# Optimization experiments

Measured on AMD Instinct MI355X. Metric: run time of the kernel, lower is better.

## Reference

```python
import jax, jax.numpy as jnp
import numpy as np

S, P, H, E = 32, 32, 128, 64        # scenes, peds/scene, h_dim, embedding_dim
B1, B2 = 512, 1024                  # mlp_pre_pool hidden, bottleneck_dim
M1 = 1024                           # decoder mlp hidden
N = S * P
T = 12                              # seq_len (decode horizon)
BN_INV = 1.0 / np.sqrt(1.0 + 1e-5)  # eval-mode BatchNorm, running mean=0 var=1


def setup_inputs() -> dict:
    key = jax.random.key(0)
    ks = jax.random.split(key, 32)
    rn = lambda k, sh, s=0.05: jax.random.normal(k, sh, dtype=jnp.float32) * s
    inp = {
        'last_pos': rn(ks[0], (N, 2), 1.0),
        'last_pos_rel': rn(ks[1], (N, 2), 1.0),
        'h0': rn(ks[2], (N, H), 0.1),
        'c0': rn(ks[3], (N, H), 0.1),
        'seq_start_end': jnp.stack([jnp.arange(S) * P, (jnp.arange(S) + 1) * P], 1).astype(jnp.int32),
        # decoder spatial embedding Linear(2, E)
        'emb_W': rn(ks[4], (E, 2)), 'emb_b': rn(ks[5], (E,)),
        # LSTM (torch gate order i,f,g,o)
        'lstm_Wih': rn(ks[6], (4 * H, E)), 'lstm_Whh': rn(ks[7], (4 * H, H)),
        'lstm_bih': rn(ks[8], (4 * H,)), 'lstm_bhh': rn(ks[9], (4 * H,)),
        # hidden2pos Linear(H, 2)
        'pos_W': rn(ks[10], (2, H)), 'pos_b': rn(ks[11], (2,)),
        # pool_net spatial embedding Linear(2, E)
        'sp_W': rn(ks[12], (E, 2)), 'sp_b': rn(ks[13], (E,)),
        # mlp_pre_pool: Linear(E+H, 512)+BN+ReLU, Linear(512, 1024)+BN+ReLU
        'pp1_W': rn(ks[14], (B1, E + H)), 'pp1_b': rn(ks[15], (B1,)),
        'pp1_g': 1.0 + rn(ks[16], (B1,)), 'pp1_be': rn(ks[17], (B1,)),
        'pp2_W': rn(ks[18], (B2, B1)), 'pp2_b': rn(ks[19], (B2,)),
        'pp2_g': 1.0 + rn(ks[20], (B2,)), 'pp2_be': rn(ks[21], (B2,)),
        # decoder mlp: Linear(H+1024, 1024)+BN+ReLU, Linear(1024, H)+BN+ReLU
        'm1_W': rn(ks[22], (M1, H + B2)), 'm1_b': rn(ks[23], (M1,)),
        'm1_g': 1.0 + rn(ks[24], (M1,)), 'm1_be': rn(ks[25], (M1,)),
        'm2_W': rn(ks[26], (H, M1)), 'm2_b': rn(ks[27], (H,)),
        'm2_g': 1.0 + rn(ks[28], (H,)), 'm2_be': rn(ks[29], (H,)),
    }
    return inp


def _bn(x, g, b):
    return x * BN_INV * g + b


def reference(last_pos, last_pos_rel, h0, c0, seq_start_end,
              emb_W, emb_b, lstm_Wih, lstm_Whh, lstm_bih, lstm_bhh,
              pos_W, pos_b, sp_W, sp_b,
              pp1_W, pp1_b, pp1_g, pp1_be, pp2_W, pp2_b, pp2_g, pp2_be,
              m1_W, m1_b, m1_g, m1_be, m2_W, m2_b, m2_g, m2_be):
    # seq_start_end encodes uniform scenes of size P; pooling is done per scene.
    def step(carry, _):
        h, c, lp, din = carry  # h,c:[N,H]  lp:[N,2]  din:[N,E]
        gates = din @ lstm_Wih.T + lstm_bih + h @ lstm_Whh.T + lstm_bhh
        i, f, g_, o = jnp.split(gates, 4, axis=-1)
        c2 = jax.nn.sigmoid(f) * c + jax.nn.sigmoid(i) * jnp.tanh(g_)
        h2 = jax.nn.sigmoid(o) * jnp.tanh(c2)
        rel_pos = h2 @ pos_W.T + pos_b          # [N,2]
        curr = rel_pos + lp                     # [N,2]
        # ---- PoolHiddenNet: per-scene all-pairs gather -> MLP -> max ----
        ps = curr.reshape(S, P, 2)
        rel = ps[:, None, :, :] - ps[:, :, None, :]   # [s,i,j] = pos_j - pos_i
        rel = rel / jnp.maximum(jnp.linalg.norm(rel, axis=-1, keepdims=True), 1e-12)
        emb = rel @ sp_W.T + sp_b                      # [S,P,P,E]
        hj = jnp.broadcast_to(h2.reshape(S, 1, P, H), (S, P, P, H))
        x = jnp.concatenate([emb, hj], -1)             # [S,P,P,E+H]
        x = jax.nn.relu(_bn(x @ pp1_W.T + pp1_b, pp1_g, pp1_be))
        x = jax.nn.relu(_bn(x @ pp2_W.T + pp2_b, pp2_g, pp2_be))
        pool = x.max(axis=2).reshape(N, B2)            # max over neighbours j
        # ---- hidden refinement MLP ----
        dh = jnp.concatenate([h2, pool], 1)
        dh = jax.nn.relu(_bn(dh @ m1_W.T + m1_b, m1_g, m1_be))
        dh = jax.nn.relu(_bn(dh @ m2_W.T + m2_b, m2_g, m2_be))
        din2 = rel_pos @ emb_W.T + emb_b
        return (dh, c2, curr, din2), rel_pos

    din0 = last_pos_rel @ emb_W.T + emb_b
    _, preds = jax.lax.scan(step, (h0, c0, last_pos, din0), None, length=T)
    return preds  # [T, N, 2] predicted relative displacements
```

## Files before the change

### kernel.cpp

```cpp
#include <hip/hip_runtime.h>
#include <hip/hip_bf16.h>
#include <math.h>

#define DEVFN __device__ __forceinline__

constexpr float BN_INV = 0.99999500003749971f;

DEVFN float sigm(float x) { return 1.0f / (1.0f + expf(-x)); }

DEVFN unsigned short f2bf(float f) {
    __hip_bfloat16 b = __float2bfloat16(f);
    return *reinterpret_cast<unsigned short*>(&b);
}
DEVFN float bf2f(unsigned short u) {
    unsigned int x = ((unsigned int)u) << 16;
    return *reinterpret_cast<float*>(&x);
}
DEVFN void splitf(float v, unsigned short& h, unsigned short& l) {
    h = f2bf(v);
    l = f2bf(v - bf2f(h));
}
DEVFN unsigned int pack2(unsigned short a, unsigned short b) {
    return (unsigned int)a | ((unsigned int)b << 16);
}
DEVFN unsigned int packsplit(float v) {
    unsigned short h, l;
    splitf(v, h, l);
    return pack2(h, l);
}

typedef __attribute__((ext_vector_type(8))) short short8;
typedef __attribute__((ext_vector_type(4))) float f32x4;

DEVFN void unzip16(unsigned short* dh, unsigned short* dl,
                   uint4 a0, uint4 a1, uint4 a2, uint4 a3) {
    uint4 h0, h1, l0, l1;
    h0.x = (a0.x & 0xffffu) | (a0.y << 16); l0.x = (a0.x >> 16) | (a0.y & 0xffff0000u);
    h0.y = (a0.z & 0xffffu) | (a0.w << 16); l0.y = (a0.z >> 16) | (a0.w & 0xffff0000u);
    h0.z = (a1.x & 0xffffu) | (a1.y << 16); l0.z = (a1.x >> 16) | (a1.y & 0xffff0000u);
    h0.w = (a1.z & 0xffffu) | (a1.w << 16); l0.w = (a1.z >> 16) | (a1.w & 0xffff0000u);
    h1.x = (a2.x & 0xffffu) | (a2.y << 16); l1.x = (a2.x >> 16) | (a2.y & 0xffff0000u);
    h1.y = (a2.z & 0xffffu) | (a2.w << 16); l1.y = (a2.z >> 16) | (a2.w & 0xffff0000u);
    h1.z = (a3.x & 0xffffu) | (a3.y << 16); l1.z = (a3.x >> 16) | (a3.y & 0xffff0000u);
    h1.w = (a3.z & 0xffffu) | (a3.w << 16); l1.w = (a3.z >> 16) | (a3.w & 0xffff0000u);
    *(uint4*)dh = h0; *(uint4*)(dh + 8) = h1;
    *(uint4*)dl = l0; *(uint4*)(dl + 8) = l1;
}

#define ASYNC_COPY16(gsrc, ldst)                                                            \
    __builtin_amdgcn_global_load_lds((const __attribute__((address_space(1))) unsigned int*)(gsrc), \
                                     (__attribute__((address_space(3))) unsigned int*)(ldst), 16, 0, 0)


__global__ void pre_misc(
    const float* __restrict__ Wih, const float* __restrict__ Whh,
    const float* __restrict__ bih, const float* __restrict__ bhh,
    float* __restrict__ WgT, float* __restrict__ bg,
    const float* __restrict__ pp1W, const float* __restrict__ pp1g,
    float* __restrict__ Wh1T,
    const float* __restrict__ spW, const float* __restrict__ spb,
    const float* __restrict__ pp1b, const float* __restrict__ pp1be,
    float* __restrict__ Mp, float* __restrict__ c1,
    const float* __restrict__ lp, const float* __restrict__ lpr,
    const float* __restrict__ h0, const float* __restrict__ c0,
    const float* __restrict__ embW, const float* __restrict__ embb,
    float* __restrict__ h_st, float* __restrict__ c_st,
    float* __restrict__ curr, float* __restrict__ din) {
    int bid = blockIdx.x, t = threadIdx.x;
    if (bid < 384) {
        int idx = bid * 256 + t;
        int k = idx >> 9, tt = idx & 511;
        WgT[idx] = (k < 64) ? Wih[tt * 64 + k] : Whh[tt * 128 + (k - 64)];
        if (idx < 512) bg[idx] = bih[idx] + bhh[idx];
    } else if (bid < 640) {
        int idx = (bid - 384) * 256 + t;
        int h = idx >> 9, k = idx & 511;
        Wh1T[idx] = pp1W[k * 192 + 64 + h] * (BN_INV * pp1g[k]);
    } else if (bid < 642) {
        int k = (bid - 640) * 256 + t;
        float m0 = 0.f, m1 = 0.f, c0v = 0.f;
        for (int e = 0; e < 64; e++) {
            float w = pp1W[k * 192 + e];
            m0 += spW[e * 2] * w; m1 += spW[e * 2 + 1] * w; c0v += spb[e] * w;
        }
        float s = BN_INV * pp1g[k];
        Mp[k] = m0 * s; Mp[512 + k] = m1 * s;
        c1[k] = (c0v + pp1b[k]) * s + pp1be[k];
    } else {
        int idx = (bid - 642) * 256 + t;
        h_st[idx] = h0[idx];
        c_st[idx] = c0[idx];
        if (idx < 1024 * 2) curr[idx] = lp[idx];
        if (idx < 1024 * 64) {
            int n = idx >> 6, e = idx & 63;
            din[idx] = fmaf(lpr[n * 2], embW[e * 2], fmaf(lpr[n * 2 + 1], embW[e * 2 + 1], embb[e]));
        }
    }
}

__global__ void pre_w(
    const float* __restrict__ pp2W, const float* __restrict__ pp2b,
    const float* __restrict__ pp2g, const float* __restrict__ pp2be,
    unsigned short* __restrict__ W2bf, float* __restrict__ c2v, int swz,
    const float* __restrict__ m1W, const float* __restrict__ m1b,
    const float* __restrict__ m1g, const float* __restrict__ m1be,
    unsigned int* __restrict__ M1p, float* __restrict__ cm1,
    const float* __restrict__ m2W, const float* __restrict__ m2b,
    const float* __restrict__ m2g, const float* __restrict__ m2be,
    unsigned int* __restrict__ M2p, float* __restrict__ cm2) {
    int bid = blockIdx.x, t = threadIdx.x;
    if (bid < 2048) {
        int idx = bid * 256 + t;
        int ko = idx >> 9, k = idx & 511;
        float s = BN_INV * pp2g[ko];
        int outk = swz ? ((k & ~63) | ((((k >> 3) & 7) ^ (ko & 7)) << 3) | (k & 7)) : k;
        W2bf[(ko << 9) + outk] = f2bf(pp2W[idx] * s);
        if (idx < 1024) c2v[idx] = pp2b[idx] * s + pp2be[idx];
    } else if (bid < 6656) {
        int idx = (bid - 2048) * 256 + t;
        int ko = idx / 1152;
        float s = BN_INV * m1g[ko];
        M1p[idx] = packsplit(m1W[idx] * s);
        if (idx < 1024) {
            float s2 = BN_INV * m1g[idx];
            cm1[idx] = m1b[idx] * s2 + m1be[idx];
        }
    } else {
        int idx = (bid - 6656) * 256 + t;
        int ko = idx >> 10;
        float s = BN_INV * m2g[ko];
        M2p[idx] = packsplit(m2W[idx] * s);
        if (idx < 128) {
            float s2 = BN_INV * m2g[idx];
            cm2[idx] = m2b[idx] * s2 + m2be[idx];
        }
    }
}


__global__ __launch_bounds__(512) void k_lstm(
    const float* __restrict__ WgT, const float* __restrict__ bg,
    float* __restrict__ h_st, float* __restrict__ c_st,
    float* __restrict__ din, float* __restrict__ curr,
    unsigned int* __restrict__ h2p,
    const float* __restrict__ posW, const float* __restrict__ posb,
    const float* __restrict__ embW, const float* __restrict__ embb,
    const float* __restrict__ Wh1T, const float* __restrict__ c1,
    float* __restrict__ Hp, int doHp,
    float* __restrict__ preds) {
    int n0 = blockIdx.x << 2;
    int t = threadIdx.x;
    __shared__ float xs[4][256];
    __shared__ float gates[4][512];
    __shared__ float h2s[4][128];
    __shared__ float rp[4][2];
#pragma unroll
    for (int u = 0; u < 2; u++) {
        int lin = t + (u << 9);
        int r = lin >> 8, k = lin & 255;
        float v = 0.f;
        if (k < 64) v = din[(n0 + r) * 64 + k];
        else if (k < 192) v = h_st[(n0 + r) * 128 + (k - 64)];
        xs[r][k] = v;
    }
    __syncthreads();
    float a0 = bg[t], a1 = a0, a2 = a0, a3 = a0;
#pragma unroll 4
    for (int k = 0; k < 192; k++) {
        float w = WgT[(k << 9) + t];
        a0 = fmaf(xs[0][k], w, a0);
        a1 = fmaf(xs[1][k], w, a1);
        a2 = fmaf(xs[2][k], w, a2);
        a3 = fmaf(xs[3][k], w, a3);
    }
    gates[0][t] = a0; gates[1][t] = a1; gates[2][t] = a2; gates[3][t] = a3;
    __syncthreads();
    {
        int r = t >> 7, hx = t & 127;
        float ig = sigm(gates[r][hx]);
        float fg = sigm(gates[r][128 + hx]);
        float gg = tanhf(gates[r][256 + hx]);
        float og = sigm(gates[r][384 + hx]);
        float c2 = fmaf(fg, c_st[(n0 + r) * 128 + hx], ig * gg);
        float h2 = og * tanhf(c2);
        c_st[(n0 + r) * 128 + hx] = c2;
        h2p[(n0 + r) * 128 + hx] = packsplit(h2);
        h2s[r][hx] = h2;
    }
    __syncthreads();
    int wv = t >> 6, l = t & 63;
    if (wv < 4) {
        float p0 = fmaf(h2s[wv][l], posW[l], h2s[wv][l + 64] * posW[l + 64]);
        float p1 = fmaf(h2s[wv][l], posW[128 + l], h2s[wv][l + 64] * posW[192 + l]);
#pragma unroll
        for (int off = 32; off > 0; off >>= 1) {
            p0 += __shfl_down(p0, off, 64);
            p1 += __shfl_down(p1, off, 64);
        }
        if (l == 0) { rp[wv][0] = p0 + posb[0]; rp[wv][1] = p1 + posb[1]; }
    }
    __syncthreads();
    if (t < 256) {
        int r = t >> 6, e = t & 63;
        float r0 = rp[r][0], r1 = rp[r][1];
        din[(n0 + r) * 64 + e] = fmaf(r0, embW[e * 2], fmaf(r1, embW[e * 2 + 1], embb[e]));
        if (e == 0) {
            preds[(n0 + r) * 2] = r0; preds[(n0 + r) * 2 + 1] = r1;
            curr[(n0 + r) * 2] += r0; curr[(n0 + r) * 2 + 1] += r1;
        }
    }
    if (doHp) {
        float cc = c1[t];
        float q0 = cc, q1 = cc, q2 = cc, q3 = cc;
#pragma unroll 4
        for (int h = 0; h < 128; h++) {
            float w = Wh1T[(h << 9) + t];
            q0 = fmaf(h2s[0][h], w, q0);
            q1 = fmaf(h2s[1][h], w, q1);
            q2 = fmaf(h2s[2][h], w, q2);
            q3 = fmaf(h2s[3][h], w, q3);
        }
        Hp[((n0 + 0) << 9) + t] = q0;
        Hp[((n0 + 1) << 9) + t] = q1;
        Hp[((n0 + 2) << 9) + t] = q2;
        Hp[((n0 + 3) << 9) + t] = q3;
    }
}

__global__ __launch_bounds__(256) void k_x1(
    const float* __restrict__ Hp, const float* __restrict__ Mp,
    const float* __restrict__ curr, unsigned short* __restrict__ x1g) {
    int bid = blockIdx.x;
    int c = bid & 7, q = bid >> 3;
    int i = q & 31, g = q >> 5;
    int s = (g << 3) + c;
    int si = (s << 5) + i;
    int t = threadIdx.x;
    __shared__ float rx[32], ry[32];
    __shared__ float m0s[512], m1s[512];
    for (int u = t; u < 512; u += 256) { m0s[u] = Mp[u]; m1s[u] = Mp[512 + u]; }
    if (t < 32) {
        int jg = (s << 5) + t;
        float dx = curr[jg * 2] - curr[si * 2];
        float dy = curr[jg * 2 + 1] - curr[si * 2 + 1];
        float den = fmaxf(sqrtf(dx * dx + dy * dy), 1e-12f);
        rx[t] = dx / den; ry[t] = dy / den;
    }
    __syncthreads();
    int j = t >> 3, c8 = t & 7;
    float rxv = rx[j], ryv = ry[j];
    const float* hp = Hp + (((s << 5) + j) << 9);
    unsigned short* op = x1g + ((size_t)((si << 5) + j) << 9);
    int swz = (c8 ^ (j & 7)) << 3;
#pragma unroll
    for (int kt = 0; kt < 512; kt += 64) {
        int k = kt + (c8 << 3);
        float4 ha = *(const float4*)(hp + k);
        float4 hb = *(const float4*)(hp + k + 4);
        uint4 o;
        o.x = pack2(f2bf(fmaxf(fmaf(rxv, m0s[k + 0], fmaf(ryv, m1s[k + 0], ha.x)), 0.f)),
                    f2bf(fmaxf(fmaf(rxv, m0s[k + 1], fmaf(ryv, m1s[k + 1], ha.y)), 0.f)));
        o.y = pack2(f2bf(fmaxf(fmaf(rxv, m0s[k + 2], fmaf(ryv, m1s[k + 2], ha.z)), 0.f)),
                    f2bf(fmaxf(fmaf(rxv, m0s[k + 3], fmaf(ryv, m1s[k + 3], ha.w)), 0.f)));
        o.z = pack2(f2bf(fmaxf(fmaf(rxv, m0s[k + 4], fmaf(ryv, m1s[k + 4], hb.x)), 0.f)),
                    f2bf(fmaxf(fmaf(rxv, m0s[k + 5], fmaf(ryv, m1s[k + 5], hb.y)), 0.f)));
        o.w = pack2(f2bf(fmaxf(fmaf(rxv, m0s[k + 6], fmaf(ryv, m1s[k + 6], hb.z)), 0.f)),
                    f2bf(fmaxf(fmaf(rxv, m0s[k + 7], fmaf(ryv, m1s[k + 7], hb.w)), 0.f)));
        *(uint4*)(op + kt + swz) = o;
    }
}

__global__ __launch_bounds__(1024, 4) void k_pool_g(
    const unsigned short* __restrict__ x1g, const unsigned short* __restrict__ W2bf,
    const float* __restrict__ c2v,
    unsigned int* __restrict__ poolp) {
    int bid = blockIdx.x;
    int c = bid & 7, q = bid >> 3;
    int inner = q & 15, g = q >> 4;
    int s = (g << 3) + c;
    int rb = inner >> 2;
    int koB = (inner & 3) << 8;
    int t = threadIdx.x;
    int lane = t & 63, wv = t >> 6;
    int quad = lane >> 4, l15 = lane & 15;
    int wr = wv >> 2, wc = wv & 3;
    int qrow = wr << 6, qcol = wc << 6;
    __shared__ unsigned short As[2][256 * 64];
    __shared__ unsigned short Bs[2][256 * 64];
    f32x4 acc[4][4];
#pragma unroll
    for (int a = 0; a < 4; a++)
#pragma unroll
        for (int b = 0; b < 4; b++) acc[a][b] = (f32x4){0.f, 0.f, 0.f, 0.f};

    int rlane = lane >> 3;
    int clane = (lane & 7) << 3;
    const unsigned short* gA = x1g + (size_t)((s << 10) + (rb << 8) + (wv << 4) + rlane) * 512 + clane;
    const unsigned short* gB = W2bf + (size_t)(koB + (wv << 4) + rlane) * 512 + clane;
    const unsigned short* pa0 = &As[0][((qrow + l15) << 6) + ((quad ^ (l15 & 7)) << 3)];
    const unsigned short* pb0 = &Bs[0][((qcol + l15) << 6) + ((quad ^ (l15 & 7)) << 3)];
    const unsigned short* pa1 = &As[0][((qrow + l15) << 6) + (((4 + quad) ^ (l15 & 7)) << 3)];
    const unsigned short* pb1 = &Bs[0][((qcol + l15) << 6) + (((4 + quad) ^ (l15 & 7)) << 3)];

#define POOL_STAGE(kt, buf)                                           \
    do {                                                              \
        unsigned short* lA = &As[buf][wv << 10];                      \
        unsigned short* lB = &Bs[buf][wv << 10];                      \
        ASYNC_COPY16(gA + (kt), lA);                                  \
        ASYNC_COPY16(gA + (kt) + 8 * 512, lA + (8 << 6));             \
        ASYNC_COPY16(gB + (kt), lB);                                  \
        ASYNC_COPY16(gB + (kt) + 8 * 512, lB + (8 << 6));             \
    } while (0)

    POOL_STAGE(0, 0);
    __syncthreads();
    for (int i = 0; i < 8; i++) {
        if (i < 7) POOL_STAGE((i + 1) << 6, (i + 1) & 1);
        int off = (i & 1) << 14;
        short8 aF[4], bF[4];
#pragma unroll
        for (int a = 0; a < 4; a++) aF[a] = *(const short8*)(pa0 + off + (a << 10));
#pragma unroll
        for (int b = 0; b < 4; b++) bF[b] = *(const short8*)(pb0 + off + (b << 10));
#pragma unroll
        for (int a = 0; a < 4; a++)
#pragma unroll
            for (int b = 0; b < 4; b++)
                acc[a][b] = __builtin_amdgcn_mfma_f32_16x16x32_bf16(aF[a], bF[b], acc[a][b], 0, 0, 0);
#pragma unroll
        for (int a = 0; a < 4; a++) aF[a] = *(const short8*)(pa1 + off + (a << 10));
#pragma unroll
        for (int b = 0; b < 4; b++) bF[b] = *(const short8*)(pb1 + off + (b << 10));
#pragma unroll
        for (int a = 0; a < 4; a++)
#pragma unroll
            for (int b = 0; b < 4; b++)
                acc[a][b] = __builtin_amdgcn_mfma_f32_16x16x32_bf16(aF[a], bF[b], acc[a][b], 0, 0, 0);
        __syncthreads();
    }
#undef POOL_STAGE

    float mx0[4], mx1[4];
#pragma unroll
    for (int b = 0; b < 4; b++) {
        float m = acc[0][b].x;
#pragma unroll
        for (int a = 0; a < 2; a++) {
            m = fmaxf(m, acc[a][b].x); m = fmaxf(m, acc[a][b].y);
            m = fmaxf(m, acc[a][b].z); m = fmaxf(m, acc[a][b].w);
        }
        m = fmaxf(m, __shfl_xor(m, 16));
        m = fmaxf(m, __shfl_xor(m, 32));
        mx0[b] = m;
        float n = acc[2][b].x;
#pragma unroll
        for (int a = 2; a < 4; a++) {
            n = fmaxf(n, acc[a][b].x); n = fmaxf(n, acc[a][b].y);
            n = fmaxf(n, acc[a][b].z); n = fmaxf(n, acc[a][b].w);
        }
        n = fmaxf(n, __shfl_xor(n, 16));
        n = fmaxf(n, __shfl_xor(n, 32));
        mx1[b] = n;
    }
    float v0 = (quad == 0) ? mx0[0] : (quad == 1) ? mx0[1] : (quad == 2) ? mx0[2] : mx0[3];
    float v1 = (quad == 0) ? mx1[0] : (quad == 1) ? mx1[1] : (quad == 2) ? mx1[2] : mx1[3];
    int col = koB + qcol + (quad << 4) + l15;
    int i0 = (rb << 3) + (wr << 1);
    int si0 = (s << 5) + i0;
    float bias = c2v[col];
    poolp[si0 * 1024 + col] = packsplit(fmaxf(v0 + bias, 0.f));
    poolp[(si0 + 1) * 1024 + col] = packsplit(fmaxf(v1 + bias, 0.f));
}

__global__ __launch_bounds__(256) void k_pool_mfma(
    const float* __restrict__ Hp, const float* __restrict__ Mp,
    const unsigned short* __restrict__ W2bf,
    const float* __restrict__ c2v, const float* __restrict__ curr,
    unsigned int* __restrict__ poolp) {
    int s = blockIdx.z;
    int rb = blockIdx.y;
    int koBase = blockIdx.x << 7;
    int t = threadIdx.x;
    int lane = t & 63, wv = t >> 6;
    int quad = lane >> 4, l15 = lane & 15;
    int qrow = (wv >> 1) << 6;
    int qcol = (wv & 1) << 6;

    __shared__ unsigned short As[128 * 40];
    __shared__ unsigned short Bs[128 * 40];
    __shared__ float rx[128], ry[128];

    if (t < 128) {
        int iL = t >> 5, j = t & 31;
        int ig = (s << 5) + (rb << 2) + iL;
        int jg = (s << 5) + j;
        float dx = curr[jg * 2] - curr[ig * 2];
        float dy = curr[jg * 2 + 1] - curr[ig * 2 + 1];
        float den = fmaxf(sqrtf(dx * dx + dy * dy), 1e-12f);
        rx[t] = dx / den; ry[t] = dy / den;
    }
    __syncthreads();

    f32x4 acc[4][4];
#pragma unroll
    for (int a = 0; a < 4; a++)
#pragma unroll
        for (int b = 0; b < 4; b++) acc[a][b] = (f32x4){0.f, 0.f, 0.f, 0.f};

    int r0 = t >> 3, c4 = (t & 7) << 2;
    int bn = t >> 1, bk = (t & 1) << 4;

    for (int kt = 0; kt < 512; kt += 32) {
#pragma unroll
        for (int p = 0; p < 4; p++) {
            int rr = r0 + (p << 5);
            int j = rr & 31;
            int kg = kt + c4;
            float4 hv = *(const float4*)(Hp + (((s << 5) + j) << 9) + kg);
            float4 m0 = *(const float4*)(Mp + kg);
            float4 m1 = *(const float4*)(Mp + 512 + kg);
            float rxv = rx[rr], ryv = ry[rr];
            float v0 = fmaxf(fmaf(rxv, m0.x, fmaf(ryv, m1.x, hv.x)), 0.f);
            float v1 = fmaxf(fmaf(rxv, m0.y, fmaf(ryv, m1.y, hv.y)), 0.f);
            float v2 = fmaxf(fmaf(rxv, m0.z, fmaf(ryv, m1.z, hv.z)), 0.f);
            float v3 = fmaxf(fmaf(rxv, m0.w, fmaf(ryv, m1.w, hv.w)), 0.f);
            unsigned int u0 = pack2(f2bf(v0), f2bf(v1));
            unsigned int u1 = pack2(f2bf(v2), f2bf(v3));
            *(uint2*)(&As[rr * 40 + c4]) = make_uint2(u0, u1);
        }
        {
            const unsigned short* src = W2bf + (((koBase + bn) << 9) + kt + bk);
            uint4 w0 = *(const uint4*)src;
            uint4 w1 = *(const uint4*)(src + 8);
            *(uint4*)(&Bs[bn * 40 + bk]) = w0;
            *(uint4*)(&Bs[bn * 40 + bk + 8]) = w1;
        }
        __syncthreads();
        short8 bF[4];
#pragma unroll
        for (int b = 0; b < 4; b++)
            bF[b] = *(const short8*)(&Bs[(qcol + (b << 4) + l15) * 40 + (quad << 3)]);
#pragma unroll
        for (int a = 0; a < 4; a++) {
            short8 aF = *(const short8*)(&As[(qrow + (a << 4) + l15) * 40 + (quad << 3)]);
#pragma unroll
            for (int b = 0; b < 4; b++)
                acc[a][b] = __builtin_amdgcn_mfma_f32_16x16x32_bf16(aF, bF[b], acc[a][b], 0, 0, 0);
        }
        __syncthreads();
    }

    float mx0[4], mx1[4];
#pragma unroll
    for (int b = 0; b < 4; b++) {
        float m = acc[0][b].x;
#pragma unroll
        for (int a = 0; a < 2; a++) {
            m = fmaxf(m, acc[a][b].x); m = fmaxf(m, acc[a][b].y);
            m = fmaxf(m, acc[a][b].z); m = fmaxf(m, acc[a][b].w);
        }
        m = fmaxf(m, __shfl_xor(m, 16));
        m = fmaxf(m, __shfl_xor(m, 32));
        mx0[b] = m;
        float n = acc[2][b].x;
#pragma unroll
        for (int a = 2; a < 4; a++) {
            n = fmaxf(n, acc[a][b].x); n = fmaxf(n, acc[a][b].y);
            n = fmaxf(n, acc[a][b].z); n = fmaxf(n, acc[a][b].w);
        }
        n = fmaxf(n, __shfl_xor(n, 16));
        n = fmaxf(n, __shfl_xor(n, 32));
        mx1[b] = n;
    }
    float v0 = (quad == 0) ? mx0[0] : (quad == 1) ? mx0[1] : (quad == 2) ? mx0[2] : mx0[3];
    float v1 = (quad == 0) ? mx1[0] : (quad == 1) ? mx1[1] : (quad == 2) ? mx1[2] : mx1[3];
    int col = koBase + qcol + (quad << 4) + l15;
    int i0 = (rb << 2) + ((wv >> 1) << 1);
    int si0 = (s << 5) + i0;
    float bias = c2v[col];
    poolp[si0 * 1024 + col] = packsplit(fmaxf(v0 + bias, 0.f));
    poolp[(si0 + 1) * 1024 + col] = packsplit(fmaxf(v1 + bias, 0.f));
}

__global__ __launch_bounds__(256) void k_m1_mfma(
    const unsigned int* __restrict__ h2p, const unsigned int* __restrict__ poolp,
    const unsigned int* __restrict__ M1p, const float* __restrict__ cm1,
    unsigned int* __restrict__ dh1p) {
    int bid = blockIdx.x;
    int c = bid & 7, q = bid >> 3;
    int kg = (c << 1) | (q >> 4);
    int rowg = q & 15;
    int rowBase = rowg << 6;
    int koBase = kg << 6;
    int t = threadIdx.x;
    int lane = t & 63, wv = t >> 6;
    int quad = lane >> 4, l15 = lane & 15;
    int qrow = (wv >> 1) << 5, qcol = (wv & 1) << 5;
    __shared__ unsigned short Ah[64 * 72], Al[64 * 72], Bh[64 * 72], Bl[64 * 72];
    f32x4 acc[2][2];
#pragma unroll
    for (int a = 0; a < 2; a++)
#pragma unroll
        for (int b = 0; b < 2; b++) acc[a][b] = (f32x4){0.f, 0.f, 0.f, 0.f};

    int ar = t >> 2, ak = (t & 3) << 4;

    for (int kt = 0; kt < 1152; kt += 64) {
        {
            const unsigned int* srcA = (kt < 128)
                ? h2p + (rowBase + ar) * 128 + kt + ak
                : poolp + (rowBase + ar) * 1024 + (kt - 128) + ak;
            uint4 a0 = ((const uint4*)srcA)[0];
            uint4 a1 = ((const uint4*)srcA)[1];
            uint4 a2 = ((const uint4*)srcA)[2];
            uint4 a3 = ((const uint4*)srcA)[3];
            const unsigned int* srcB = M1p + (koBase + ar) * 1152 + kt + ak;
            uint4 b0 = ((const uint4*)srcB)[0];
            uint4 b1 = ((const uint4*)srcB)[1];
            uint4 b2 = ((const uint4*)srcB)[2];
            uint4 b3 = ((const uint4*)srcB)[3];
            unzip16(&Ah[ar * 72 + ak], &Al[ar * 72 + ak], a0, a1, a2, a3);
            unzip16(&Bh[ar * 72 + ak], &Bl[ar * 72 + ak], b0, b1, b2, b3);
        }
        __syncthreads();
#pragma unroll
        for (int kk2 = 0; kk2 < 2; kk2++) {
            int kc = ((kk2 << 2) | quad) << 3;
            short8 bH[2], bL[2];
#pragma unroll
            for (int b = 0; b < 2; b++) {
                int boff = (qcol + (b << 4) + l15) * 72 + kc;
                bH[b] = *(const short8*)(&Bh[boff]);
                bL[b] = *(const short8*)(&Bl[boff]);
            }
#pragma unroll
            for (int a = 0; a < 2; a++) {
                int aoff = (qrow + (a << 4) + l15) * 72 + kc;
                short8 aH = *(const short8*)(&Ah[aoff]);
                short8 aL = *(const short8*)(&Al[aoff]);
#pragma unroll
                for (int b = 0; b < 2; b++) {
                    acc[a][b] = __builtin_amdgcn_mfma_f32_16x16x32_bf16(aH, bH[b], acc[a][b], 0, 0, 0);
                    acc[a][b] = __builtin_amdgcn_mfma_f32_16x16x32_bf16(aH, bL[b], acc[a][b], 0, 0, 0);
                    acc[a][b] = __builtin_amdgcn_mfma_f32_16x16x32_bf16(aL, bH[b], acc[a][b], 0, 0, 0);
                }
            }
        }
        __syncthreads();
    }
#pragma unroll
    for (int b = 0; b < 2; b++) {
        int col = koBase + qcol + (b << 4) + l15;
        float bias = cm1[col];
#pragma unroll
        for (int a = 0; a < 2; a++) {
#pragma unroll
            for (int rg = 0; rg < 4; rg++) {
                int row = rowBase + qrow + (a << 4) + (quad << 2) + rg;
                dh1p[row * 1024 + col] = packsplit(fmaxf(acc[a][b][rg] + bias, 0.f));
            }
        }
    }
}

__global__ __launch_bounds__(256) void k_m2_mfma(
    const unsigned int* __restrict__ dh1p, const unsigned int* __restrict__ M2p,
    const float* __restrict__ cm2, float* __restrict__ h_st) {
    int rowBase = blockIdx.x << 5;
    int t = threadIdx.x;
    int lane = t & 63, wv = t >> 6;
    int quad = lane >> 4, l15 = lane & 15;
    int qrow = (wv >> 1) << 4;
    int qcol = (wv & 1) << 6;
    __shared__ unsigned short Ah[32 * 40], Al[32 * 40], Bh[128 * 40], Bl[128 * 40];
    f32x4 acc[4];
#pragma unroll
    for (int b = 0; b < 4; b++) acc[b] = (f32x4){0.f, 0.f, 0.f, 0.f};

    int ar = t >> 3, ak = (t & 7) << 2;
    int br = t >> 1, bk = (t & 1) << 4;

    for (int kt = 0; kt < 1024; kt += 32) {
        {
            uint4 av = *(const uint4*)(dh1p + (rowBase + ar) * 1024 + kt + ak);
            uint2 hi = make_uint2((av.x & 0xffffu) | (av.y << 16),
                                  (av.z & 0xffffu) | (av.w << 16));
            uint2 lo = make_uint2((av.x >> 16) | (av.y & 0xffff0000u),
                                  (av.z >> 16) | (av.w & 0xffff0000u));
            *(uint2*)&Ah[ar * 40 + ak] = hi;
            *(uint2*)&Al[ar * 40 + ak] = lo;
        }
        {
            const unsigned int* srcB = M2p + br * 1024 + kt + bk;
            uint4 b0 = ((const uint4*)srcB)[0];
            uint4 b1 = ((const uint4*)srcB)[1];
            uint4 b2 = ((const uint4*)srcB)[2];
            uint4 b3 = ((const uint4*)srcB)[3];
            unzip16(&Bh[br * 40 + bk], &Bl[br * 40 + bk], b0, b1, b2, b3);
        }
        __syncthreads();
        {
            int aoff = (qrow + l15) * 40 + (quad << 3);
            short8 aH = *(const short8*)(&Ah[aoff]);
            short8 aL = *(const short8*)(&Al[aoff]);
#pragma unroll
            for (int b = 0; b < 4; b++) {
                int boff = (qcol + (b << 4) + l15) * 40 + (quad << 3);
                short8 bH = *(const short8*)(&Bh[boff]);
                short8 bL = *(const short8*)(&Bl[boff]);
                acc[b] = __builtin_amdgcn_mfma_f32_16x16x32_bf16(aH, bH, acc[b], 0, 0, 0);
                acc[b] = __builtin_amdgcn_mfma_f32_16x16x32_bf16(aH, bL, acc[b], 0, 0, 0);
                acc[b] = __builtin_amdgcn_mfma_f32_16x16x32_bf16(aL, bH, acc[b], 0, 0, 0);
            }
        }
        __syncthreads();
    }
#pragma unroll
    for (int b = 0; b < 4; b++) {
        int col = qcol + (b << 4) + l15;
        float bias = cm2[col];
#pragma unroll
        for (int rg = 0; rg < 4; rg++) {
            int row = rowBase + qrow + (quad << 2) + rg;
            h_st[row * 128 + col] = fmaxf(acc[b][rg] + bias, 0.f);
        }
    }
}


extern "C" void kernel_launch(void* const* d_in, const int* in_sizes, int n_in,
                              void* d_out, int out_size, void* d_ws, size_t ws_size,
                              hipStream_t stream) {
    const float* last_pos     = (const float*)d_in[0];
    const float* last_pos_rel = (const float*)d_in[1];
    const float* h0   = (const float*)d_in[2];
    const float* c0   = (const float*)d_in[3];
    const float* emb_W = (const float*)d_in[5];
    const float* emb_b = (const float*)d_in[6];
    const float* lstm_Wih = (const float*)d_in[7];
    const float* lstm_Whh = (const float*)d_in[8];
    const float* lstm_bih = (const float*)d_in[9];
    const float* lstm_bhh = (const float*)d_in[10];
    const float* pos_W = (const float*)d_in[11];
    const float* pos_b = (const float*)d_in[12];
    const float* sp_W  = (const float*)d_in[13];
    const float* sp_b  = (const float*)d_in[14];
    const float* pp1_W = (const float*)d_in[15];
    const float* pp1_b = (const float*)d_in[16];
    const float* pp1_g = (const float*)d_in[17];
    const float* pp1_be= (const float*)d_in[18];
    const float* pp2_W = (const float*)d_in[19];
    const float* pp2_b = (const float*)d_in[20];
    const float* pp2_g = (const float*)d_in[21];
    const float* pp2_be= (const float*)d_in[22];
    const float* m1_W  = (const float*)d_in[23];
    const float* m1_b  = (const float*)d_in[24];
    const float* m1_g  = (const float*)d_in[25];
    const float* m1_be = (const float*)d_in[26];
    const float* m2_W  = (const float*)d_in[27];
    const float* m2_b  = (const float*)d_in[28];
    const float* m2_g  = (const float*)d_in[29];
    const float* m2_be = (const float*)d_in[30];
    float* out = (float*)d_out;

    float* p = (float*)d_ws;
    float* WgT  = p; p += 192 * 512;
    float* bg   = p; p += 512;
    float* Wh1T = p; p += 128 * 512;
    float* Mp   = p; p += 2 * 512;
    float* c1   = p; p += 512;
    unsigned short* W2bf = (unsigned short*)p; p += 512 * 1024 / 2;
    float* c2v  = p; p += 1024;
    unsigned int* M1p = (unsigned int*)p; p += 1024 * 1152;
    float* cm1  = p; p += 1024;
    unsigned int* M2p = (unsigned int*)p; p += 128 * 1024;
    float* cm2  = p; p += 128;
    float* h_st = p; p += 1024 * 128;
    float* c_st = p; p += 1024 * 128;
    unsigned int* h2p = (unsigned int*)p; p += 1024 * 128;
    float* curr = p; p += 1024 * 2;
    float* din  = p; p += 1024 * 64;
    float* Hp   = p; p += 1024 * 512;
    unsigned int* poolp = (unsigned int*)p; p += 1024 * 1024;
    unsigned int* dh1p = (unsigned int*)p; p += 1024 * 1024;
    unsigned short* x1g = (unsigned short*)p;
    size_t need = (size_t)((char*)(x1g + (size_t)32768 * 512) - (char*)d_ws);
    int big = (ws_size >= need) ? 1 : 0;

    pre_misc<<<1154, 256, 0, stream>>>(lstm_Wih, lstm_Whh, lstm_bih, lstm_bhh, WgT, bg,
                                       pp1_W, pp1_g, Wh1T,
                                       sp_W, sp_b, pp1_b, pp1_be, Mp, c1,
                                       last_pos, last_pos_rel, h0, c0, emb_W, emb_b,
                                       h_st, c_st, curr, din);
    pre_w<<<7168, 256, 0, stream>>>(pp2_W, pp2_b, pp2_g, pp2_be, W2bf, c2v, big,
                                    m1_W, m1_b, m1_g, m1_be, M1p, cm1,
                                    m2_W, m2_b, m2_g, m2_be, M2p, cm2);

    for (int t = 0; t < 12; t++) {
        k_lstm<<<256, 512, 0, stream>>>(WgT, bg, h_st, c_st, din, curr, h2p,
                                        pos_W, pos_b, emb_W, emb_b,
                                        Wh1T, c1, Hp, (t < 11) ? 1 : 0, out + t * 2048);
        if (t == 11) break;
        if (big) {
            k_x1<<<1024, 256, 0, stream>>>(Hp, Mp, curr, x1g);
            k_pool_g<<<512, 1024, 0, stream>>>(x1g, W2bf, c2v, poolp);
        } else {
            k_pool_mfma<<<dim3(8, 8, 32), 256, 0, stream>>>(Hp, Mp, W2bf, c2v, curr, poolp);
        }
        k_m1_mfma<<<256, 256, 0, stream>>>(h2p, poolp, M1p, cm1, dh1p);
        k_m2_mfma<<<32, 256, 0, stream>>>(dh1p, M2p, cm2, h_st);
    }
}
```

Baseline: 1.484 ms.

## Fuse pairwise first-layer activation build into pooled GEMM kernel

Removes the separate k_x1 kernel that materialised the full bf16 pairwise activation tensor in global memory, and instead builds each A tile from Hp, Mp and relative positions inside the pool GEMM while B tiles are fetched asynchronously. This avoids writing and then re-reading a large intermediate each step, at the cost of ALU work and global reads inside the GEMM main loop that are not overlapped by async copies. The fallback small-workspace path is dropped, and the m1 kernel grid is changed from a swizzled 1D mapping to a plain 2D grid.

```diff
diff --git a/kernel.cpp b/kernel.cpp
--- a/kernel.cpp
+++ b/kernel.cpp
@@ -101,7 +101,7 @@
 __global__ void pre_w(
     const float* __restrict__ pp2W, const float* __restrict__ pp2b,
     const float* __restrict__ pp2g, const float* __restrict__ pp2be,
-    unsigned short* __restrict__ W2bf, float* __restrict__ c2v, int swz,
+    unsigned short* __restrict__ W2bf, float* __restrict__ c2v,
     const float* __restrict__ m1W, const float* __restrict__ m1b,
     const float* __restrict__ m1g, const float* __restrict__ m1be,
     unsigned int* __restrict__ M1p, float* __restrict__ cm1,
@@ -113,7 +113,7 @@
         int idx = bid * 256 + t;
         int ko = idx >> 9, k = idx & 511;
         float s = BN_INV * pp2g[ko];
-        int outk = swz ? ((k & ~63) | ((((k >> 3) & 7) ^ (ko & 7)) << 3) | (k & 7)) : k;
+        int outk = (k & ~63) | ((((k >> 3) & 7) ^ (ko & 7)) << 3) | (k & 7);
         W2bf[(ko << 9) + outk] = f2bf(pp2W[idx] * s);
         if (idx < 1024) c2v[idx] = pp2b[idx] * s + pp2be[idx];
     } else if (bid < 6656) {
@@ -227,51 +227,9 @@
     }
 }
 
-__global__ __launch_bounds__(256) void k_x1(
+__global__ __launch_bounds__(1024, 4) void k_pool_f(
     const float* __restrict__ Hp, const float* __restrict__ Mp,
-    const float* __restrict__ curr, unsigned short* __restrict__ x1g) {
-    int bid = blockIdx.x;
-    int c = bid & 7, q = bid >> 3;
-    int i = q & 31, g = q >> 5;
-    int s = (g << 3) + c;
-    int si = (s << 5) + i;
-    int t = threadIdx.x;
-    __shared__ float rx[32], ry[32];
-    __shared__ float m0s[512], m1s[512];
-    for (int u = t; u < 512; u += 256) { m0s[u] = Mp[u]; m1s[u] = Mp[512 + u]; }
-    if (t < 32) {
-        int jg = (s << 5) + t;
-        float dx = curr[jg * 2] - curr[si * 2];
-        float dy = curr[jg * 2 + 1] - curr[si * 2 + 1];
-        float den = fmaxf(sqrtf(dx * dx + dy * dy), 1e-12f);
-        rx[t] = dx / den; ry[t] = dy / den;
-    }
-    __syncthreads();
-    int j = t >> 3, c8 = t & 7;
-    float rxv = rx[j], ryv = ry[j];
-    const float* hp = Hp + (((s << 5) + j) << 9);
-    unsigned short* op = x1g + ((size_t)((si << 5) + j) << 9);
-    int swz = (c8 ^ (j & 7)) << 3;
-#pragma unroll
-    for (int kt = 0; kt < 512; kt += 64) {
-        int k = kt + (c8 << 3);
-        float4 ha = *(const float4*)(hp + k);
-        float4 hb = *(const float4*)(hp + k + 4);
-        uint4 o;
-        o.x = pack2(f2bf(fmaxf(fmaf(rxv, m0s[k + 0], fmaf(ryv, m1s[k + 0], ha.x)), 0.f)),
-                    f2bf(fmaxf(fmaf(rxv, m0s[k + 1], fmaf(ryv, m1s[k + 1], ha.y)), 0.f)));
-        o.y = pack2(f2bf(fmaxf(fmaf(rxv, m0s[k + 2], fmaf(ryv, m1s[k + 2], ha.z)), 0.f)),
-                    f2bf(fmaxf(fmaf(rxv, m0s[k + 3], fmaf(ryv, m1s[k + 3], ha.w)), 0.f)));
-        o.z = pack2(f2bf(fmaxf(fmaf(rxv, m0s[k + 4], fmaf(ryv, m1s[k + 4], hb.x)), 0.f)),
-                    f2bf(fmaxf(fmaf(rxv, m0s[k + 5], fmaf(ryv, m1s[k + 5], hb.y)), 0.f)));
-        o.w = pack2(f2bf(fmaxf(fmaf(rxv, m0s[k + 6], fmaf(ryv, m1s[k + 6], hb.z)), 0.f)),
-                    f2bf(fmaxf(fmaf(rxv, m0s[k + 7], fmaf(ryv, m1s[k + 7], hb.w)), 0.f)));
-        *(uint4*)(op + kt + swz) = o;
-    }
-}
-
-__global__ __launch_bounds__(1024, 4) void k_pool_g(
-    const unsigned short* __restrict__ x1g, const unsigned short* __restrict__ W2bf,
+    const float* __restrict__ curr, const unsigned short* __restrict__ W2bf,
     const float* __restrict__ c2v,
     unsigned int* __restrict__ poolp) {
     int bid = blockIdx.x;
@@ -287,35 +245,95 @@
     int qrow = wr << 6, qcol = wc << 6;
     __shared__ unsigned short As[2][256 * 64];
     __shared__ unsigned short Bs[2][256 * 64];
+    __shared__ float rxs[256], rys[256];
+
+    if (t < 256) {
+        int iL = t >> 5, j = t & 31;
+        int ig = (s << 5) + (rb << 3) + iL;
+        int jg = (s << 5) + j;
+        float dx = curr[jg * 2] - curr[ig * 2];
+        float dy = curr[jg * 2 + 1] - curr[ig * 2 + 1];
+        float den = fmaxf(sqrtf(dx * dx + dy * dy), 1e-12f);
+        rxs[t] = dx / den; rys[t] = dy / den;
+    }
+    __syncthreads();
+
     f32x4 acc[4][4];
 #pragma unroll
     for (int a = 0; a < 4; a++)
 #pragma unroll
         for (int b = 0; b < 4; b++) acc[a][b] = (f32x4){0.f, 0.f, 0.f, 0.f};
+
+    int br_ = t >> 2;
+    int bj = br_ & 31;
+    int k0 = (t & 3) << 4;
+    int c0 = (t & 3) << 1;
+    int sw0 = ((c0 ^ (br_ & 7)) << 3);
+    int sw1 = (((c0 + 1) ^ (br_ & 7)) << 3);
+    const float* hpRow = Hp + (((s << 5) + bj) << 9);
+    float rxv = rxs[br_], ryv = rys[br_];
 
     int rlane = lane >> 3;
     int clane = (lane & 7) << 3;
-    const unsigned short* gA = x1g + (size_t)((s << 10) + (rb << 8) + (wv << 4) + rlane) * 512 + clane;
     const unsigned short* gB = W2bf + (size_t)(koB + (wv << 4) + rlane) * 512 + clane;
+
     const unsigned short* pa0 = &As[0][((qrow + l15) << 6) + ((quad ^ (l15 & 7)) << 3)];
     const unsigned short* pb0 = &Bs[0][((qcol + l15) << 6) + ((quad ^ (l15 & 7)) << 3)];
     const unsigned short* pa1 = &As[0][((qrow + l15) << 6) + (((4 + quad) ^ (l15 & 7)) << 3)];
     const unsigned short* pb1 = &Bs[0][((qcol + l15) << 6) + (((4 + quad) ^ (l15 & 7)) << 3)];
 
-#define POOL_STAGE(kt, buf)                                           \
+#define BUILD_A(kt, buf)                                                        \
+    do {                                                                        \
+        unsigned short* baseA = &As[buf][br_ << 6];                             \
+        int kk = (kt) + k0;                                                     \
+        float4 h0 = *(const float4*)(hpRow + kk);                               \
+        float4 h1 = *(const float4*)(hpRow + kk + 4);                           \
+        float4 h2v = *(const float4*)(hpRow + kk + 8);                          \
+        float4 h3 = *(const float4*)(hpRow + kk + 12);                          \
+        float4 p0 = *(const float4*)(Mp + kk);                                  \
+        float4 p1 = *(const float4*)(Mp + kk + 4);                              \
+        float4 p2 = *(const float4*)(Mp + kk + 8);                              \
+        float4 p3 = *(const float4*)(Mp + kk + 12);                             \
+        float4 q0 = *(const float4*)(Mp + 512 + kk);                            \
+        float4 q1 = *(const float4*)(Mp + 512 + kk + 4);                        \
+        float4 q2 = *(const float4*)(Mp + 512 + kk + 8);                        \
+        float4 q3 = *(const float4*)(Mp + 512 + kk + 12);                       \
+        uint4 o0, o1;                                                           \
+        o0.x = pack2(f2bf(fmaxf(fmaf(rxv, p0.x, fmaf(ryv, q0.x, h0.x)), 0.f)),  \
+                     f2bf(fmaxf(fmaf(rxv, p0.y, fmaf(ryv, q0.y, h0.y)), 0.f))); \
+        o0.y = pack2(f2bf(fmaxf(fmaf(rxv, p0.z, fmaf(ryv, q0.z, h0.z)), 0.f)),  \
+                     f2bf(fmaxf(fmaf(rxv, p0.w, fmaf(ryv, q0.w, h0.w)), 0.f))); \
+        o0.z = pack2(f2bf(fmaxf(fmaf(rxv, p1.x, fmaf(ryv, q1.x, h1.x)), 0.f)),  \
+                     f2bf(fmaxf(fmaf(rxv, p1.y, fmaf(ryv, q1.y, h1.y)), 0.f))); \
+        o0.w = pack2(f2bf(fmaxf(fmaf(rxv, p1.z, fmaf(ryv, q1.z, h1.z)), 0.f)),  \
+                     f2bf(fmaxf(fmaf(rxv, p1.w, fmaf(ryv, q1.w, h1.w)), 0.f))); \
+        o1.x = pack2(f2bf(fmaxf(fmaf(rxv, p2.x, fmaf(ryv, q2.x, h2v.x)), 0.f)), \
+                     f2bf(fmaxf(fmaf(rxv, p2.y, fmaf(ryv, q2.y, h2v.y)), 0.f))); \
+        o1.y = pack2(f2bf(fmaxf(fmaf(rxv, p2.z, fmaf(ryv, q2.z, h2v.z)), 0.f)), \
+                     f2bf(fmaxf(fmaf(rxv, p2.w, fmaf(ryv, q2.w, h2v.w)), 0.f))); \
+        o1.z = pack2(f2bf(fmaxf(fmaf(rxv, p3.x, fmaf(ryv, q3.x, h3.x)), 0.f)),  \
+                     f2bf(fmaxf(fmaf(rxv, p3.y, fmaf(ryv, q3.y, h3.y)), 0.f))); \
+        o1.w = pack2(f2bf(fmaxf(fmaf(rxv, p3.z, fmaf(ryv, q3.z, h3.z)), 0.f)),  \
+                     f2bf(fmaxf(fmaf(rxv, p3.w, fmaf(ryv, q3.w, h3.w)), 0.f))); \
+        *(uint4*)(baseA + sw0) = o0;                                            \
+        *(uint4*)(baseA + sw1) = o1;                                            \
+    } while (0)
+
+#define STAGE_B(kt, buf)                                              \
     do {                                                              \
-        unsigned short* lA = &As[buf][wv << 10];                      \
         unsigned short* lB = &Bs[buf][wv << 10];                      \
-        ASYNC_COPY16(gA + (kt), lA);                                  \
-        ASYNC_COPY16(gA + (kt) + 8 * 512, lA + (8 << 6));             \
         ASYNC_COPY16(gB + (kt), lB);                                  \
         ASYNC_COPY16(gB + (kt) + 8 * 512, lB + (8 << 6));             \
     } while (0)
 
-    POOL_STAGE(0, 0);
+    STAGE_B(0, 0);
+    BUILD_A(0, 0);
     __syncthreads();
     for (int i = 0; i < 8; i++) {
-        if (i < 7) POOL_STAGE((i + 1) << 6, (i + 1) & 1);
+        if (i < 7) {
+            STAGE_B((i + 1) << 6, (i + 1) & 1);
+            BUILD_A((i + 1) << 6, (i + 1) & 1);
+        }
         int off = (i & 1) << 14;
         short8 aF[4], bF[4];
 #pragma unroll
@@ -338,7 +356,8 @@
                 acc[a][b] = __builtin_amdgcn_mfma_f32_16x16x32_bf16(aF[a], bF[b], acc[a][b], 0, 0, 0);
         __syncthreads();
     }
-#undef POOL_STAGE
+#undef BUILD_A
+#undef STAGE_B
 
     float mx0[4], mx1[4];
 #pragma unroll
@@ -372,126 +391,12 @@
     poolp[(si0 + 1) * 1024 + col] = packsplit(fmaxf(v1 + bias, 0.f));
 }
 
-__global__ __launch_bounds__(256) void k_pool_mfma(
-    const float* __restrict__ Hp, const float* __restrict__ Mp,
-    const unsigned short* __restrict__ W2bf,
-    const float* __restrict__ c2v, const float* __restrict__ curr,
-    unsigned int* __restrict__ poolp) {
-    int s = blockIdx.z;
-    int rb = blockIdx.y;
-    int koBase = blockIdx.x << 7;
-    int t = threadIdx.x;
-    int lane = t & 63, wv = t >> 6;
-    int quad = lane >> 4, l15 = lane & 15;
-    int qrow = (wv >> 1) << 6;
-    int qcol = (wv & 1) << 6;
-
-    __shared__ unsigned short As[128 * 40];
-    __shared__ unsigned short Bs[128 * 40];
-    __shared__ float rx[128], ry[128];
-
-    if (t < 128) {
-        int iL = t >> 5, j = t & 31;
-        int ig = (s << 5) + (rb << 2) + iL;
-        int jg = (s << 5) + j;
-        float dx = curr[jg * 2] - curr[ig * 2];
-        float dy = curr[jg * 2 + 1] - curr[ig * 2 + 1];
-        float den = fmaxf(sqrtf(dx * dx + dy * dy), 1e-12f);
-        rx[t] = dx / den; ry[t] = dy / den;
-    }
-    __syncthreads();
-
-    f32x4 acc[4][4];
-#pragma unroll
-    for (int a = 0; a < 4; a++)
-#pragma unroll
-        for (int b = 0; b < 4; b++) acc[a][b] = (f32x4){0.f, 0.f, 0.f, 0.f};
-
-    int r0 = t >> 3, c4 = (t & 7) << 2;
-    int bn = t >> 1, bk = (t & 1) << 4;
-
-    for (int kt = 0; kt < 512; kt += 32) {
-#pragma unroll
-        for (int p = 0; p < 4; p++) {
-            int rr = r0 + (p << 5);
-            int j = rr & 31;
-            int kg = kt + c4;
-            float4 hv = *(const float4*)(Hp + (((s << 5) + j) << 9) + kg);
-            float4 m0 = *(const float4*)(Mp + kg);
-            float4 m1 = *(const float4*)(Mp + 512 + kg);
-            float rxv = rx[rr], ryv = ry[rr];
-            float v0 = fmaxf(fmaf(rxv, m0.x, fmaf(ryv, m1.x, hv.x)), 0.f);
-            float v1 = fmaxf(fmaf(rxv, m0.y, fmaf(ryv, m1.y, hv.y)), 0.f);
-            float v2 = fmaxf(fmaf(rxv, m0.z, fmaf(ryv, m1.z, hv.z)), 0.f);
-            float v3 = fmaxf(fmaf(rxv, m0.w, fmaf(ryv, m1.w, hv.w)), 0.f);
-            unsigned int u0 = pack2(f2bf(v0), f2bf(v1));
-            unsigned int u1 = pack2(f2bf(v2), f2bf(v3));
-            *(uint2*)(&As[rr * 40 + c4]) = make_uint2(u0, u1);
-        }
-        {
-            const unsigned short* src = W2bf + (((koBase + bn) << 9) + kt + bk);
-            uint4 w0 = *(const uint4*)src;
-            uint4 w1 = *(const uint4*)(src + 8);
-            *(uint4*)(&Bs[bn * 40 + bk]) = w0;
-            *(uint4*)(&Bs[bn * 40 + bk + 8]) = w1;
-        }
-        __syncthreads();
-        short8 bF[4];
-#pragma unroll
-        for (int b = 0; b < 4; b++)
-            bF[b] = *(const short8*)(&Bs[(qcol + (b << 4) + l15) * 40 + (quad << 3)]);
-#pragma unroll
-        for (int a = 0; a < 4; a++) {
-            short8 aF = *(const short8*)(&As[(qrow + (a << 4) + l15) * 40 + (quad << 3)]);
-#pragma unroll
-            for (int b = 0; b < 4; b++)
-                acc[a][b] = __builtin_amdgcn_mfma_f32_16x16x32_bf16(aF, bF[b], acc[a][b], 0, 0, 0);
-        }
-        __syncthreads();
-    }
-
-    float mx0[4], mx1[4];
-#pragma unroll
-    for (int b = 0; b < 4; b++) {
-        float m = acc[0][b].x;
-#pragma unroll
-        for (int a = 0; a < 2; a++) {
-            m = fmaxf(m, acc[a][b].x); m = fmaxf(m, acc[a][b].y);
-            m = fmaxf(m, acc[a][b].z); m = fmaxf(m, acc[a][b].w);
-        }
-        m = fmaxf(m, __shfl_xor(m, 16));
-        m = fmaxf(m, __shfl_xor(m, 32));
-        mx0[b] = m;
-        float n = acc[2][b].x;
-#pragma unroll
-        for (int a = 2; a < 4; a++) {
-            n = fmaxf(n, acc[a][b].x); n = fmaxf(n, acc[a][b].y);
-            n = fmaxf(n, acc[a][b].z); n = fmaxf(n, acc[a][b].w);
-        }
-        n = fmaxf(n, __shfl_xor(n, 16));
-        n = fmaxf(n, __shfl_xor(n, 32));
-        mx1[b] = n;
-    }
-    float v0 = (quad == 0) ? mx0[0] : (quad == 1) ? mx0[1] : (quad == 2) ? mx0[2] : mx0[3];
-    float v1 = (quad == 0) ? mx1[0] : (quad == 1) ? mx1[1] : (quad == 2) ? mx1[2] : mx1[3];
-    int col = koBase + qcol + (quad << 4) + l15;
-    int i0 = (rb << 2) + ((wv >> 1) << 1);
-    int si0 = (s << 5) + i0;
-    float bias = c2v[col];
-    poolp[si0 * 1024 + col] = packsplit(fmaxf(v0 + bias, 0.f));
-    poolp[(si0 + 1) * 1024 + col] = packsplit(fmaxf(v1 + bias, 0.f));
-}
-
 __global__ __launch_bounds__(256) void k_m1_mfma(
     const unsigned int* __restrict__ h2p, const unsigned int* __restrict__ poolp,
     const unsigned int* __restrict__ M1p, const float* __restrict__ cm1,
     unsigned int* __restrict__ dh1p) {
-    int bid = blockIdx.x;
-    int c = bid & 7, q = bid >> 3;
-    int kg = (c << 1) | (q >> 4);
-    int rowg = q & 15;
-    int rowBase = rowg << 6;
-    int koBase = kg << 6;
+    int rowBase = blockIdx.y << 6;
+    int koBase = blockIdx.x << 6;
     int t = threadIdx.x;
     int lane = t & 63, wv = t >> 6;
     int quad = lane >> 4, l15 = lane & 15;
@@ -683,16 +588,13 @@
     float* Hp   = p; p += 1024 * 512;
     unsigned int* poolp = (unsigned int*)p; p += 1024 * 1024;
     unsigned int* dh1p = (unsigned int*)p; p += 1024 * 1024;
-    unsigned short* x1g = (unsigned short*)p;
-    size_t need = (size_t)((char*)(x1g + (size_t)32768 * 512) - (char*)d_ws);
-    int big = (ws_size >= need) ? 1 : 0;
 
     pre_misc<<<1154, 256, 0, stream>>>(lstm_Wih, lstm_Whh, lstm_bih, lstm_bhh, WgT, bg,
                                        pp1_W, pp1_g, Wh1T,
                                        sp_W, sp_b, pp1_b, pp1_be, Mp, c1,
                                        last_pos, last_pos_rel, h0, c0, emb_W, emb_b,
                                        h_st, c_st, curr, din);
-    pre_w<<<7168, 256, 0, stream>>>(pp2_W, pp2_b, pp2_g, pp2_be, W2bf, c2v, big,
+    pre_w<<<7168, 256, 0, stream>>>(pp2_W, pp2_b, pp2_g, pp2_be, W2bf, c2v,
                                     m1_W, m1_b, m1_g, m1_be, M1p, cm1,
                                     m2_W, m2_b, m2_g, m2_be, M2p, cm2);
 
@@ -701,13 +603,8 @@
                                         pos_W, pos_b, emb_W, emb_b,
                                         Wh1T, c1, Hp, (t < 11) ? 1 : 0, out + t * 2048);
         if (t == 11) break;
-        if (big) {
-            k_x1<<<1024, 256, 0, stream>>>(Hp, Mp, curr, x1g);
-            k_pool_g<<<512, 1024, 0, stream>>>(x1g, W2bf, c2v, poolp);
-        } else {
-            k_pool_mfma<<<dim3(8, 8, 32), 256, 0, stream>>>(Hp, Mp, W2bf, c2v, curr, poolp);
-        }
-        k_m1_mfma<<<256, 256, 0, stream>>>(h2p, poolp, M1p, cm1, dh1p);
+        k_pool_f<<<512, 1024, 0, stream>>>(Hp, Mp, curr, W2bf, c2v, poolp);
+        k_m1_mfma<<<dim3(16, 16), 256, 0, stream>>>(h2p, poolp, M1p, cm1, dh1p);
         k_m2_mfma<<<32, 256, 0, stream>>>(dh1p, M2p, cm2, h_st);
     }
 }
```

Result: slower. 1.821 ms (+22.7%).
